# Kernel optimization log

Measured on AMD Instinct MI355X. Metric: run time of the kernel, lower is better.

## Reference

```python
import jax, jax.numpy as jnp
import numpy as np

B, S, T, D, H, HD = 1, 2048, 256, 3072, 24, 128
FF = 4 * D
EPS_LN = 1e-6
EPS_RMS = 1e-6


def _layernorm(x):
    m = jnp.mean(x, axis=-1, keepdims=True)
    v = jnp.mean(jnp.square(x - m), axis=-1, keepdims=True)
    return (x - m) * jax.lax.rsqrt(v + EPS_LN)


def _rmsnorm(x, w):
    return x * jax.lax.rsqrt(jnp.mean(jnp.square(x), axis=-1, keepdims=True) + EPS_RMS) * w


def _rope_interleaved(x, cos, sin):
    # x: [B,S,H,HD], cos/sin: [S,HD//2]; non-neox (interleaved) style
    x1 = x[..., 0::2]
    x2 = x[..., 1::2]
    c = cos[None, :, None, :]
    s = sin[None, :, None, :]
    o1 = x1 * c - x2 * s
    o2 = x2 * c + x1 * s
    return jnp.stack([o1, o2], axis=-1).reshape(x.shape)


def setup_inputs() -> dict:
    key = jax.random.key(0)
    ks = jax.random.split(key, 12)

    def n(k, shape, scale):
        return jax.random.normal(k, shape, dtype=jnp.float32) * scale

    # real RoPE tables
    pos = np.arange(S, dtype=np.float64)
    inv_freq = 1.0 / (10000.0 ** (np.arange(0, HD, 2, dtype=np.float64) / HD))
    ang = np.outer(pos, inv_freq)  # [S, HD//2]

    return {
        "img": n(ks[0], (B, S, D), 1.0),
        "vec": n(ks[1], (B, D), 1.0),
        "cos": jnp.asarray(np.cos(ang), jnp.float32),
        "sin": jnp.asarray(np.sin(ang), jnp.float32),
        "k_txt": n(ks[2], (B, T, H, HD), 1.0),
        "v_txt": n(ks[3], (B, T, H, HD), 1.0),
        "mod_w": n(ks[4], (D, 6 * D), 0.02),
        "mod_b": jnp.zeros((6 * D,), jnp.float32),
        "qkv_w": n(ks[5], (D, 3 * D), 0.02),
        "qkv_b": jnp.zeros((3 * D,), jnp.float32),
        "qn_w": jnp.ones((HD,), jnp.float32),
        "kn_w": jnp.ones((HD,), jnp.float32),
        "proj_w": n(ks[6], (D, D), 0.02),
        "proj_b": jnp.zeros((D,), jnp.float32),
        "mlp_w1": n(ks[7], (D, FF), 0.02),
        "mlp_b1": jnp.zeros((FF,), jnp.float32),
        "mlp_w2": n(ks[8], (FF, D), 0.02),
        "mlp_b2": jnp.zeros((D,), jnp.float32),
    }


def reference(img, vec, cos, sin, k_txt, v_txt, mod_w, mod_b, qkv_w, qkv_b,
              qn_w, kn_w, proj_w, proj_b, mlp_w1, mlp_b1, mlp_w2, mlp_b2):
    # modulation: silu(vec) -> linear -> 6 chunks, each [B,1,D]
    mod = jax.nn.silu(vec) @ mod_w + mod_b
    (a_shift, a_scale, a_gate, m_shift, m_scale, m_gate) = [
        m[:, None, :] for m in jnp.split(mod, 6, axis=-1)
    ]

    # LayerNorm (no affine) + scale/shift modulate
    x = _layernorm(img) * (1.0 + a_scale) + a_shift

    qkv = (x @ qkv_w + qkv_b).reshape(B, S, 3, H, HD)
    q, k, v = qkv[:, :, 0], qkv[:, :, 1], qkv[:, :, 2]
    q = _rmsnorm(q, qn_w)
    k = _rmsnorm(k, kn_w)
    q = _rope_interleaved(q, cos, sin)
    k = _rope_interleaved(k, cos, sin)

    # concat text KV cache (no RoPE on text tokens)
    k_all = jnp.concatenate([k, k_txt], axis=1)  # [B,S+T,H,HD]
    v_all = jnp.concatenate([v, v_txt], axis=1)

    scale = 1.0 / jnp.sqrt(jnp.asarray(HD, jnp.float32))
    scores = jnp.einsum('bqhd,bkhd->bhqk', q, k_all) * scale
    probs = jax.nn.softmax(scores, axis=-1)
    attn = jnp.einsum('bhqk,bkhd->bqhd', probs, v_all).reshape(B, S, D)

    attn_out = attn @ proj_w + proj_b

    # ScaleResidualLayerNormScaleShift
    residual = img + a_gate * attn_out
    mlp_in = _layernorm(residual) * (1.0 + m_scale) + m_shift

    mlp_out = jax.nn.gelu(mlp_in @ mlp_w1 + mlp_b1, approximate=True) @ mlp_w2 + mlp_b2
    return residual + m_gate * mlp_out
```

## Files before the change

kernel.cpp:

```cpp
#include <hip/hip_runtime.h>

typedef short short8 __attribute__((ext_vector_type(8)));
typedef float f32x4 __attribute__((ext_vector_type(4)));

#define DEV static __device__ __forceinline__

DEV unsigned short f2bf(float f) {
  union { float f; unsigned u; } v; v.f = f;
  unsigned u = v.u;
  unsigned r = u + 0x7fffu + ((u >> 16) & 1u);
  return (unsigned short)(r >> 16);
}
DEV float bf2f(unsigned short b) {
  union { unsigned u; float f; } v; v.u = ((unsigned)b) << 16;
  return v.f;
}
DEV void load_lds16(const void* g, void* l) {
  __builtin_amdgcn_global_load_lds(
      (const __attribute__((address_space(1))) unsigned int*)g,
      (__attribute__((address_space(3))) unsigned int*)l, 16, 0, 0);
}
DEV int swz(int L) { return L ^ ((L >> 3) & 0x30); }

__global__ __launch_bounds__(256) void zero_mod(const float* __restrict__ b, float* __restrict__ out) {
  int j = blockIdx.x * 256 + threadIdx.x;
  out[j] = b[j];
}

__global__ __launch_bounds__(256) void mod_gemv(const float* __restrict__ vec,
                                                const float* __restrict__ W,
                                                float* __restrict__ out) {
  __shared__ float sv[192];
  int tid = threadIdx.x;
  int kb = blockIdx.y * 192;
  if (tid < 192) {
    float x = vec[kb + tid];
    sv[tid] = x / (1.f + __expf(-x));
  }
  __syncthreads();
  int j = blockIdx.x * 256 + tid;
  float a0 = 0, a1 = 0, a2 = 0, a3 = 0;
  for (int i = 0; i < 192; i += 4) {
    a0 += sv[i + 0] * W[(size_t)(kb + i + 0) * 18432 + j];
    a1 += sv[i + 1] * W[(size_t)(kb + i + 1) * 18432 + j];
    a2 += sv[i + 2] * W[(size_t)(kb + i + 2) * 18432 + j];
    a3 += sv[i + 3] * W[(size_t)(kb + i + 3) * 18432 + j];
  }
  atomicAdd(&out[j], a0 + a1 + a2 + a3);
}

__global__ __launch_bounds__(256) void ln_kernel(const float* __restrict__ in,
                                                 const float* __restrict__ mod,
                                                 int shift_off, int scale_off,
                                                 unsigned short* __restrict__ out) {
  int rowb = blockIdx.x;
  const float* x = in + (size_t)rowb * 3072;
  int tid = threadIdx.x;
  float s = 0.f, ss = 0.f;
  float4 v[3];
#pragma unroll
  for (int r = 0; r < 3; r++) {
    v[r] = *(const float4*)&x[r * 1024 + tid * 4];
    s += v[r].x + v[r].y + v[r].z + v[r].w;
    ss += v[r].x * v[r].x + v[r].y * v[r].y + v[r].z * v[r].z + v[r].w * v[r].w;
  }
#pragma unroll
  for (int m = 32; m; m >>= 1) { s += __shfl_xor(s, m); ss += __shfl_xor(ss, m); }
  __shared__ float red[8];
  int w = tid >> 6, lane = tid & 63;
  if (lane == 0) { red[w] = s; red[4 + w] = ss; }
  __syncthreads();
  s = red[0] + red[1] + red[2] + red[3];
  ss = red[4] + red[5] + red[6] + red[7];
  float mean = s * (1.f / 3072.f);
  float var = ss * (1.f / 3072.f) - mean * mean;
  float rstd = rsqrtf(var + 1e-6f);
#pragma unroll
  for (int r = 0; r < 3; r++) {
    int c = r * 1024 + tid * 4;
    float xv[4] = {v[r].x, v[r].y, v[r].z, v[r].w};
#pragma unroll
    for (int i = 0; i < 4; i++) {
      float o = (xv[i] - mean) * rstd * (1.f + mod[scale_off + c + i]) + mod[shift_off + c + i];
      out[(size_t)rowb * 3072 + c + i] = f2bf(o);
    }
  }
}

__global__ __launch_bounds__(256) void transpose_k(const float* __restrict__ src,
                                                   unsigned short* __restrict__ dst,
                                                   int K, int N) {
  __shared__ float t[64][65];
  int n0 = blockIdx.x * 64, k0 = blockIdx.y * 64;
  int tid = threadIdx.x;
#pragma unroll
  for (int i = 0; i < 16; i++) {
    int lin = i * 256 + tid;
    int r = lin >> 6, c = lin & 63;
    t[r][c] = src[(size_t)(k0 + r) * N + n0 + c];
  }
  __syncthreads();
#pragma unroll
  for (int i = 0; i < 16; i++) {
    int lin = i * 256 + tid;
    int rn = lin >> 6, cn = lin & 63;
    dst[(size_t)(n0 + rn) * K + k0 + cn] = f2bf(t[cn][rn]);
  }
}

__global__ __launch_bounds__(256) void vt_k(const unsigned short* __restrict__ qkvb,
                                            const float* __restrict__ v_txt,
                                            unsigned short* __restrict__ vt) {
  int h = blockIdx.y;
  int c8 = blockIdx.x * 2 + (threadIdx.x >> 7);
  int d = threadIdx.x & 127;
  int kvb = c8 * 8;
  short8 o;
  if (kvb < 2048) {
#pragma unroll
    for (int j = 0; j < 8; j++)
      o[j] = (short)qkvb[(size_t)(kvb + j) * 9216 + 6144 + h * 128 + d];
  } else {
#pragma unroll
    for (int j = 0; j < 8; j++)
      o[j] = (short)f2bf(v_txt[((size_t)(kvb + j - 2048) * 24 + h) * 128 + d]);
  }
  *(short8*)&vt[((size_t)h * 128 + d) * 2304 + kvb] = o;
}

template <int EPI>
__global__ __launch_bounds__(512, 2) void gemm8(const unsigned short* __restrict__ A,
                                                const unsigned short* __restrict__ Bt,
                                                const float* __restrict__ bias,
                                                unsigned short* __restrict__ outb,
                                                int N, int ldk, int klen) {
  __shared__ unsigned short As[4][8192];
  __shared__ unsigned short Bs[4][8192];
  const int tid = threadIdx.x, lane = tid & 63, w = tid >> 6;
  const int wr = w >> 2, wc = w & 3;
  const int lr = lane & 15, lk = lane >> 4;

  const int bm = blockIdx.y * 256, bn = blockIdx.x * 256;
  const int kbase = blockIdx.z * klen;
  const int NT = klen >> 5;

  const int D0 = tid * 16;
  const int D1 = 8192 + tid * 16;
  const int L0 = swz(D0), L1 = swz(D1);
  const unsigned short* sA0 = A + (size_t)(bm + (L0 >> 6)) * ldk + kbase + ((L0 & 63) >> 1);
  const unsigned short* sA1 = A + (size_t)(bm + (L1 >> 6)) * ldk + kbase + ((L1 & 63) >> 1);
  const unsigned short* sB0 = Bt + (size_t)(bn + (L0 >> 6)) * ldk + kbase + ((L0 & 63) >> 1);
  const unsigned short* sB1 = Bt + (size_t)(bn + (L1 >> 6)) * ldk + kbase + ((L1 & 63) >> 1);

  int aoff[8], boff[4];
#pragma unroll
  for (int mi = 0; mi < 8; mi++)
    aoff[mi] = swz(((wr * 128 + mi * 16 + lr) << 6) | (lk << 4));
#pragma unroll
  for (int ni = 0; ni < 4; ni++)
    boff[ni] = swz(((wc * 64 + ni * 16 + lr) << 6) | (lk << 4));

  f32x4 acc[8][4];
#pragma unroll
  for (int i = 0; i < 8; i++)
#pragma unroll
    for (int j = 0; j < 4; j++) acc[i][j] = (f32x4){0.f, 0.f, 0.f, 0.f};

#pragma unroll
  for (int j = 0; j < 3; j++) {
    load_lds16(sA0 + j * 32, (char*)As + j * 16384 + D0);
    load_lds16(sA1 + j * 32, (char*)As + j * 16384 + D1);
    load_lds16(sB0 + j * 32, (char*)Bs + j * 16384 + D0);
    load_lds16(sB1 + j * 32, (char*)Bs + j * 16384 + D1);
  }
  asm volatile("s_waitcnt vmcnt(8)" ::: "memory");
  __builtin_amdgcn_sched_barrier(0);
  __builtin_amdgcn_s_barrier();

  for (int t = 0; t < NT; ++t) {
    const int rt = t & 3;
    char* Ab = (char*)As + rt * 16384;
    char* Bb = (char*)Bs + rt * 16384;
    const int ss = (t + 3) & 3;
    const int sk = (t + 3) * 32;
    const bool stg = (t + 3) < NT;

    short8 af[8], bf[4];
#pragma unroll
    for (int mi = 0; mi < 8; mi++) af[mi] = *(const short8*)(Ab + aoff[mi]);
#pragma unroll
    for (int ni = 0; ni < 4; ni++) bf[ni] = *(const short8*)(Bb + boff[ni]);
    if (stg) {
      load_lds16(sA0 + sk, (char*)As + ss * 16384 + D0);
      load_lds16(sA1 + sk, (char*)As + ss * 16384 + D1);
      load_lds16(sB0 + sk, (char*)Bs + ss * 16384 + D0);
      load_lds16(sB1 + sk, (char*)Bs + ss * 16384 + D1);
    }
    __builtin_amdgcn_s_setprio(1);
#pragma unroll
    for (int mi = 0; mi < 8; mi++)
#pragma unroll
      for (int ni = 0; ni < 4; ni++)
        acc[mi][ni] = __builtin_amdgcn_mfma_f32_16x16x32_bf16(af[mi], bf[ni], acc[mi][ni], 0, 0, 0);
    __builtin_amdgcn_s_setprio(0);
    if (t < NT - 3) {
      asm volatile("s_waitcnt vmcnt(8)" ::: "memory");
    } else if (t == NT - 3) {
      asm volatile("s_waitcnt vmcnt(4)" ::: "memory");
    } else if (t == NT - 2) {
      asm volatile("s_waitcnt vmcnt(0)" ::: "memory");
    }
    __builtin_amdgcn_sched_barrier(0);
    __builtin_amdgcn_s_barrier();
  }

  const size_t zoff = (size_t)blockIdx.z * ((size_t)2048 * N);
#pragma unroll
  for (int mi = 0; mi < 8; mi++) {
#pragma unroll
    for (int ni = 0; ni < 4; ni++) {
      int row0 = bm + wr * 128 + mi * 16 + lk * 4;
      int col = bn + wc * 64 + ni * 16 + lr;
#pragma unroll
      for (int r = 0; r < 4; r++) {
        float vv = acc[mi][ni][r];
        if (EPI == 0) {
          outb[(size_t)(row0 + r) * N + col] = f2bf(vv + bias[col]);
        } else if (EPI == 2) {
          float x = vv + bias[col];
          float y = 0.7978845608028654f * (x + 0.044715f * x * x * x);
          float th = 1.f - 2.f / (__expf(2.f * y) + 1.f);
          outb[(size_t)(row0 + r) * N + col] = f2bf(0.5f * x * (1.f + th));
        } else {
          outb[zoff + (size_t)(row0 + r) * N + col] = f2bf(vv);
        }
      }
    }
  }
}

__global__ __launch_bounds__(256) void sk_epi(const unsigned short* __restrict__ pb,
                                              const float* __restrict__ bias,
                                              const float* __restrict__ addsrc,
                                              const float* __restrict__ gate,
                                              float* __restrict__ out) {
  const int N = 3072;
  const size_t MN = (size_t)2048 * 3072;
  int row = blockIdx.y;
  int col = blockIdx.x * 1024 + threadIdx.x * 4;
  size_t idx = (size_t)row * N + col;
  const unsigned short* p0 = pb + idx;
  const unsigned short* p1 = pb + MN + idx;
  float4 a = *(const float4*)(addsrc + idx);
  float4 b = *(const float4*)(bias + col);
  float4 g = *(const float4*)(gate + col);
  float4 o;
  o.x = a.x + g.x * (bf2f(p0[0]) + bf2f(p1[0]) + b.x);
  o.y = a.y + g.y * (bf2f(p0[1]) + bf2f(p1[1]) + b.y);
  o.z = a.z + g.z * (bf2f(p0[2]) + bf2f(p1[2]) + b.z);
  o.w = a.w + g.w * (bf2f(p0[3]) + bf2f(p1[3]) + b.w);
  *(float4*)(out + idx) = o;
}

__global__ __launch_bounds__(64) void qkv_post(const unsigned short* __restrict__ qkv,
                                               const float* __restrict__ k_txt,
                                               const float* __restrict__ cosb,
                                               const float* __restrict__ sinb,
                                               const float* __restrict__ qn,
                                               const float* __restrict__ kn,
                                               unsigned short* __restrict__ qb,
                                               unsigned short* __restrict__ kb) {
  int s = blockIdx.x, h = blockIdx.y;
  int lane = threadIdx.x;
  int d0 = lane * 2;
  if (s < 2048) {
    const unsigned short* rowp = qkv + (size_t)s * 9216;
    float c = cosb[s * 64 + lane], sn = sinb[s * 64 + lane];
    const float ascale = 0.08838834764831845f;
    {
      float a = bf2f(rowp[h * 128 + d0]), b = bf2f(rowp[h * 128 + d0 + 1]);
      float sq = a * a + b * b;
#pragma unroll
      for (int m = 32; m; m >>= 1) sq += __shfl_xor(sq, m);
      float rr = rsqrtf(sq * (1.f / 128.f) + 1e-6f);
      float x1 = a * rr * qn[d0], x2 = b * rr * qn[d0 + 1];
      float o1 = (x1 * c - x2 * sn) * ascale;
      float o2 = (x2 * c + x1 * sn) * ascale;
      size_t off = ((size_t)h * 2048 + s) * 128 + d0;
      qb[off] = f2bf(o1); qb[off + 1] = f2bf(o2);
    }
    {
      float a = bf2f(rowp[3072 + h * 128 + d0]), b = bf2f(rowp[3072 + h * 128 + d0 + 1]);
      float sq = a * a + b * b;
#pragma unroll
      for (int m = 32; m; m >>= 1) sq += __shfl_xor(sq, m);
      float rr = rsqrtf(sq * (1.f / 128.f) + 1e-6f);
      float x1 = a * rr * kn[d0], x2 = b * rr * kn[d0 + 1];
      float o1 = x1 * c - x2 * sn;
      float o2 = x2 * c + x1 * sn;
      size_t off = ((size_t)h * 2304 + s) * 128 + d0;
      kb[off] = f2bf(o1); kb[off + 1] = f2bf(o2);
    }
  } else {
    int t = s - 2048;
    size_t src = ((size_t)t * 24 + h) * 128 + d0;
    size_t off = ((size_t)h * 2304 + s) * 128 + d0;
    kb[off] = f2bf(k_txt[src]); kb[off + 1] = f2bf(k_txt[src + 1]);
  }
}

__global__ __launch_bounds__(512) void attn_k(const unsigned short* __restrict__ qb,
                                              const unsigned short* __restrict__ kb,
                                              const unsigned short* __restrict__ vt,
                                              unsigned short* __restrict__ out) {
  __shared__ unsigned short Ks[2][8192];
  __shared__ unsigned short Vs[2][8192];
  __shared__ unsigned short Ps[8][32 * 72];
  int h = blockIdx.y, q0 = blockIdx.x * 256;
  int tid = threadIdx.x, lane = tid & 63, w = tid >> 6;
  int lr = lane & 15, lk = lane >> 4;

  const unsigned short* kh = kb + (size_t)h * 2304 * 128;
  const unsigned short* vth = vt + (size_t)h * 128 * 2304;

  short8 qf[2][4];
#pragma unroll
  for (int mi = 0; mi < 2; mi++)
#pragma unroll
    for (int kf = 0; kf < 4; kf++)
      qf[mi][kf] = *(const short8*)&qb[((size_t)h * 2048 + q0 + w * 32 + mi * 16 + lr) * 128 + kf * 32 + lk * 8];

  const int kR0 = (tid * 16) >> 8, kR1 = (tid * 16 + 8192) >> 8;
  const int kCc = ((tid * 16) >> 4) & 15;
  const int kOf0 = kR0 * 128 + ((kCc ^ (kR0 & 15)) * 8);
  const int kOf1 = kR1 * 128 + ((kCc ^ (kR1 & 15)) * 8);
  const int vR0 = (tid * 16) >> 7, vR1 = (tid * 16 + 8192) >> 7;
  const int vCc = ((tid * 16) >> 4) & 7;
  const int vOf0 = vR0 * 2304 + ((vCc ^ (vR0 & 7)) * 8);
  const int vOf1 = vR1 * 2304 + ((vCc ^ (vR1 & 7)) * 8);

  float mrow[2][4], lsum[2][4];
#pragma unroll
  for (int mi = 0; mi < 2; mi++)
#pragma unroll
    for (int r = 0; r < 4; r++) { mrow[mi][r] = -1e30f; lsum[mi][r] = 0.f; }
  f32x4 oacc[2][8];
#pragma unroll
  for (int mi = 0; mi < 2; mi++)
#pragma unroll
    for (int i = 0; i < 8; i++) oacc[mi][i] = (f32x4){0.f, 0.f, 0.f, 0.f};

  load_lds16(kh + kOf0, (char*)Ks[0] + tid * 16);
  load_lds16(kh + kOf1, (char*)Ks[0] + tid * 16 + 8192);
  load_lds16(vth + vOf0, (char*)Vs[0] + tid * 16);
  load_lds16(vth + vOf1, (char*)Vs[0] + tid * 16 + 8192);
  asm volatile("s_waitcnt vmcnt(0)" ::: "memory");
  __builtin_amdgcn_sched_barrier(0);
  __builtin_amdgcn_s_barrier();

  for (int kt = 0; kt < 36; kt++) {
    const int cur = kt & 1, nxt = cur ^ 1;
    if (kt + 1 < 36) {
      int kv1 = (kt + 1) * 64;
      load_lds16(kh + (size_t)kv1 * 128 + kOf0, (char*)Ks[nxt] + tid * 16);
      load_lds16(kh + (size_t)kv1 * 128 + kOf1, (char*)Ks[nxt] + tid * 16 + 8192);
      load_lds16(vth + kv1 + vOf0, (char*)Vs[nxt] + tid * 16);
      load_lds16(vth + kv1 + vOf1, (char*)Vs[nxt] + tid * 16 + 8192);
    }

    f32x4 sa[2][4];
#pragma unroll
    for (int mi = 0; mi < 2; mi++)
#pragma unroll
      for (int ni = 0; ni < 4; ni++) sa[mi][ni] = (f32x4){0.f, 0.f, 0.f, 0.f};
    __builtin_amdgcn_s_setprio(1);
#pragma unroll
    for (int kf = 0; kf < 4; kf++) {
#pragma unroll
      for (int ni = 0; ni < 4; ni++) {
        int n = ni * 16 + lr;
        short8 bfr = *(const short8*)&Ks[cur][n * 128 + (((kf * 4 + lk) ^ lr) & 15) * 8];
        sa[0][ni] = __builtin_amdgcn_mfma_f32_16x16x32_bf16(qf[0][kf], bfr, sa[0][ni], 0, 0, 0);
        sa[1][ni] = __builtin_amdgcn_mfma_f32_16x16x32_bf16(qf[1][kf], bfr, sa[1][ni], 0, 0, 0);
      }
    }
    __builtin_amdgcn_s_setprio(0);

#pragma unroll
    for (int mi = 0; mi < 2; mi++) {
#pragma unroll
      for (int r = 0; r < 4; r++) {
        float mx = fmaxf(fmaxf(sa[mi][0][r], sa[mi][1][r]), fmaxf(sa[mi][2][r], sa[mi][3][r]));
#pragma unroll
        for (int m = 8; m; m >>= 1) mx = fmaxf(mx, __shfl_xor(mx, m));
        float mnew = fmaxf(mrow[mi][r], mx);
        float p0 = __expf(sa[mi][0][r] - mnew);
        float p1 = __expf(sa[mi][1][r] - mnew);
        float p2 = __expf(sa[mi][2][r] - mnew);
        float p3 = __expf(sa[mi][3][r] - mnew);
        float su = p0 + p1 + p2 + p3;
#pragma unroll
        for (int m = 8; m; m >>= 1) su += __shfl_xor(su, m);
        float alpha = __expf(mrow[mi][r] - mnew);
        lsum[mi][r] = lsum[mi][r] * alpha + su;
        mrow[mi][r] = mnew;
#pragma unroll
        for (int df = 0; df < 8; df++) oacc[mi][df][r] *= alpha;
        int prow = (mi * 16 + lk * 4 + r) * 72;
        Ps[w][prow + 0 * 16 + lr] = f2bf(p0);
        Ps[w][prow + 1 * 16 + lr] = f2bf(p1);
        Ps[w][prow + 2 * 16 + lr] = f2bf(p2);
        Ps[w][prow + 3 * 16 + lr] = f2bf(p3);
      }
    }

    __builtin_amdgcn_s_setprio(1);
#pragma unroll
    for (int kf2 = 0; kf2 < 2; kf2++) {
      short8 pa0 = *(const short8*)&Ps[w][(0 * 16 + lr) * 72 + kf2 * 32 + lk * 8];
      short8 pa1 = *(const short8*)&Ps[w][(1 * 16 + lr) * 72 + kf2 * 32 + lk * 8];
#pragma unroll
      for (int df = 0; df < 8; df++) {
        int d = df * 16 + lr;
        short8 bv = *(const short8*)&Vs[cur][d * 64 + (((kf2 * 4 + lk) ^ (lr & 7)) & 7) * 8];
        oacc[0][df] = __builtin_amdgcn_mfma_f32_16x16x32_bf16(pa0, bv, oacc[0][df], 0, 0, 0);
        oacc[1][df] = __builtin_amdgcn_mfma_f32_16x16x32_bf16(pa1, bv, oacc[1][df], 0, 0, 0);
      }
    }
    __builtin_amdgcn_s_setprio(0);

    asm volatile("s_waitcnt vmcnt(0)" ::: "memory");
    __builtin_amdgcn_sched_barrier(0);
    __builtin_amdgcn_s_barrier();
  }

#pragma unroll
  for (int mi = 0; mi < 2; mi++) {
#pragma unroll
    for (int r = 0; r < 4; r++) {
      float inv = 1.f / lsum[mi][r];
      int row = q0 + w * 32 + mi * 16 + lk * 4 + r;
#pragma unroll
      for (int df = 0; df < 8; df++)
        out[(size_t)row * 3072 + h * 128 + df * 16 + lr] = f2bf(oacc[mi][df][r] * inv);
    }
  }
}

extern "C" void kernel_launch(void* const* d_in, const int* in_sizes, int n_in,
                              void* d_out, int out_size, void* d_ws, size_t ws_size,
                              hipStream_t stream) {
  const float* img = (const float*)d_in[0];
  const float* vec = (const float*)d_in[1];
  const float* cosb = (const float*)d_in[2];
  const float* sinb = (const float*)d_in[3];
  const float* k_txt = (const float*)d_in[4];
  const float* v_txt = (const float*)d_in[5];
  const float* mod_w = (const float*)d_in[6];
  const float* mod_b = (const float*)d_in[7];
  const float* qkv_w = (const float*)d_in[8];
  const float* qkv_b = (const float*)d_in[9];
  const float* qn_w = (const float*)d_in[10];
  const float* kn_w = (const float*)d_in[11];
  const float* proj_w = (const float*)d_in[12];
  const float* proj_b = (const float*)d_in[13];
  const float* mlp_w1 = (const float*)d_in[14];
  const float* mlp_b1 = (const float*)d_in[15];
  const float* mlp_w2 = (const float*)d_in[16];
  const float* mlp_b2 = (const float*)d_in[17];
  float* outp = (float*)d_out;

  char* ws = (char*)d_ws;
  unsigned short* qkvb = (unsigned short*)(ws + 0);
  unsigned short* qbuf = (unsigned short*)(ws + 37748736);
  unsigned short* kbuf = (unsigned short*)(ws + 50331648);
  unsigned short* vtbuf = (unsigned short*)(ws + 64487424);
  unsigned short* attnb = (unsigned short*)(ws + 78643200);
  float* resid = (float*)(ws + 91226112);
  unsigned short* xln = (unsigned short*)(ws + 116391936);
  float* modv = (float*)(ws + 128974848);
  unsigned short* wt = (unsigned short*)(ws + 129048576);
  unsigned short* hbuf = (unsigned short*)(ws + 0);
  unsigned short* pbuf = (unsigned short*)(ws + 50331648);

  zero_mod<<<72, 256, 0, stream>>>(mod_b, modv);
  mod_gemv<<<dim3(72, 16), 256, 0, stream>>>(vec, mod_w, modv);

  ln_kernel<<<2048, 256, 0, stream>>>(img, modv, 0, 3072, xln);

  transpose_k<<<dim3(144, 48), 256, 0, stream>>>(qkv_w, wt, 3072, 9216);
  gemm8<0><<<dim3(36, 8, 1), 512, 0, stream>>>(xln, wt, qkv_b, qkvb, 9216, 3072, 3072);

  qkv_post<<<dim3(2304, 24), 64, 0, stream>>>(qkvb, k_txt, cosb, sinb, qn_w, kn_w, qbuf, kbuf);
  vt_k<<<dim3(144, 24), 256, 0, stream>>>(qkvb, v_txt, vtbuf);

  attn_k<<<dim3(8, 24), 512, 0, stream>>>(qbuf, kbuf, vtbuf, attnb);

  transpose_k<<<dim3(48, 48), 256, 0, stream>>>(proj_w, wt, 3072, 3072);
  gemm8<3><<<dim3(12, 8, 2), 512, 0, stream>>>(attnb, wt, nullptr, pbuf, 3072, 3072, 1536);
  sk_epi<<<dim3(3, 2048), 256, 0, stream>>>(pbuf, proj_b, img, modv + 2 * 3072, resid);

  ln_kernel<<<2048, 256, 0, stream>>>(resid, modv, 3 * 3072, 4 * 3072, xln);

  transpose_k<<<dim3(192, 48), 256, 0, stream>>>(mlp_w1, wt, 3072, 12288);
  gemm8<2><<<dim3(48, 8, 1), 512, 0, stream>>>(xln, wt, mlp_b1, hbuf, 12288, 3072, 3072);

  transpose_k<<<dim3(48, 192), 256, 0, stream>>>(mlp_w2, wt, 12288, 3072);
  gemm8<3><<<dim3(12, 8, 2), 512, 0, stream>>>(hbuf, wt, nullptr, pbuf, 3072, 12288, 6144);
  sk_epi<<<dim3(3, 2048), 256, 0, stream>>>(pbuf, mlp_b2, resid, modv + 5 * 3072, outp);
}
```

Measured before the change: 958.2 us.

## Double-buffer GEMM fragments in registers to overlap LDS reads with MFMA

Restructures the gemm8 main loop into a two-step unrolled pipeline. It keeps two sets of A/B fragment registers and reads the next tile's fragments from LDS while the MFMAs for the current tile run. Prefetch issue and vmcnt waits are reorganised so each tile only waits on the tile it needs next. The aim is to hide LDS read latency behind matrix-core work. The cost is extra fragment VGPRs, which could cause spills or lower occupancy under the 512x2 launch bounds. The loop also assumes an even tile count.

```diff
diff --git a/kernel.cpp b/kernel.cpp
--- a/kernel.cpp
+++ b/kernel.cpp
@@ -127,6 +127,48 @@
   }
   *(short8*)&vt[((size_t)h * 128 + d) * 2304 + kvb] = o;
 }
+
+#define RD_FRAGS(AF, BF, Ab, Bb)                                   \
+  do {                                                             \
+    _Pragma("unroll")                                              \
+    for (int mi = 0; mi < 8; mi++) AF[mi] = *(const short8*)((Ab) + aoff[mi]); \
+    _Pragma("unroll")                                              \
+    for (int ni = 0; ni < 4; ni++) BF[ni] = *(const short8*)((Bb) + boff[ni]); \
+  } while (0)
+
+#define DO_MFMA(AF, BF)                                            \
+  do {                                                             \
+    __builtin_amdgcn_s_setprio(1);                                 \
+    _Pragma("unroll")                                              \
+    for (int mi = 0; mi < 8; mi++)                                 \
+      _Pragma("unroll")                                            \
+      for (int ni = 0; ni < 4; ni++)                               \
+        acc[mi][ni] = __builtin_amdgcn_mfma_f32_16x16x32_bf16(AF[mi], BF[ni], acc[mi][ni], 0, 0, 0); \
+    __builtin_amdgcn_s_setprio(0);                                 \
+  } while (0)
+
+#define STAGE4(TT)                                                 \
+  do {                                                             \
+    if ((TT) < NT) {                                               \
+      const int ss_ = (TT) & 3;                                    \
+      const int sk_ = (TT) * 32;                                   \
+      load_lds16(sA0 + sk_, (char*)As + ss_ * 16384 + D0);         \
+      load_lds16(sA1 + sk_, (char*)As + ss_ * 16384 + D1);         \
+      load_lds16(sB0 + sk_, (char*)Bs + ss_ * 16384 + D0);         \
+      load_lds16(sB1 + sk_, (char*)Bs + ss_ * 16384 + D1);         \
+    }                                                              \
+  } while (0)
+
+#define TILE_WAIT(U)                                               \
+  do {                                                             \
+    if ((U) <= NT - 4) {                                           \
+      asm volatile("s_waitcnt vmcnt(4)" ::: "memory");             \
+    } else {                                                       \
+      asm volatile("s_waitcnt vmcnt(0)" ::: "memory");             \
+    }                                                              \
+    __builtin_amdgcn_sched_barrier(0);                             \
+    __builtin_amdgcn_s_barrier();                                  \
+  } while (0)
 
 template <int EPI>
 __global__ __launch_bounds__(512, 2) void gemm8(const unsigned short* __restrict__ A,
@@ -166,52 +208,35 @@
 #pragma unroll
     for (int j = 0; j < 4; j++) acc[i][j] = (f32x4){0.f, 0.f, 0.f, 0.f};
 
-#pragma unroll
-  for (int j = 0; j < 3; j++) {
-    load_lds16(sA0 + j * 32, (char*)As + j * 16384 + D0);
-    load_lds16(sA1 + j * 32, (char*)As + j * 16384 + D1);
-    load_lds16(sB0 + j * 32, (char*)Bs + j * 16384 + D0);
-    load_lds16(sB1 + j * 32, (char*)Bs + j * 16384 + D1);
-  }
-  asm volatile("s_waitcnt vmcnt(8)" ::: "memory");
+  STAGE4(0);
+  STAGE4(1);
+  STAGE4(2);
+  asm volatile("s_waitcnt vmcnt(4)" ::: "memory");
   __builtin_amdgcn_sched_barrier(0);
   __builtin_amdgcn_s_barrier();
 
-  for (int t = 0; t < NT; ++t) {
-    const int rt = t & 3;
-    char* Ab = (char*)As + rt * 16384;
-    char* Bb = (char*)Bs + rt * 16384;
-    const int ss = (t + 3) & 3;
-    const int sk = (t + 3) * 32;
-    const bool stg = (t + 3) < NT;
-
-    short8 af[8], bf[4];
-#pragma unroll
-    for (int mi = 0; mi < 8; mi++) af[mi] = *(const short8*)(Ab + aoff[mi]);
-#pragma unroll
-    for (int ni = 0; ni < 4; ni++) bf[ni] = *(const short8*)(Bb + boff[ni]);
-    if (stg) {
-      load_lds16(sA0 + sk, (char*)As + ss * 16384 + D0);
-      load_lds16(sA1 + sk, (char*)As + ss * 16384 + D1);
-      load_lds16(sB0 + sk, (char*)Bs + ss * 16384 + D0);
-      load_lds16(sB1 + sk, (char*)Bs + ss * 16384 + D1);
-    }
-    __builtin_amdgcn_s_setprio(1);
-#pragma unroll
-    for (int mi = 0; mi < 8; mi++)
-#pragma unroll
-      for (int ni = 0; ni < 4; ni++)
-        acc[mi][ni] = __builtin_amdgcn_mfma_f32_16x16x32_bf16(af[mi], bf[ni], acc[mi][ni], 0, 0, 0);
-    __builtin_amdgcn_s_setprio(0);
-    if (t < NT - 3) {
-      asm volatile("s_waitcnt vmcnt(8)" ::: "memory");
-    } else if (t == NT - 3) {
-      asm volatile("s_waitcnt vmcnt(4)" ::: "memory");
-    } else if (t == NT - 2) {
-      asm volatile("s_waitcnt vmcnt(0)" ::: "memory");
-    }
-    __builtin_amdgcn_sched_barrier(0);
-    __builtin_amdgcn_s_barrier();
+  short8 afA[8], bfA[4], afB[8], bfB[4];
+  RD_FRAGS(afA, bfA, (char*)As, (char*)Bs);
+
+  for (int t = 0; t < NT; t += 2) {
+    {
+      STAGE4(t + 3);
+      char* Ab = (char*)As + ((t + 1) & 3) * 16384;
+      char* Bb = (char*)Bs + ((t + 1) & 3) * 16384;
+      RD_FRAGS(afB, bfB, Ab, Bb);
+      DO_MFMA(afA, bfA);
+      TILE_WAIT(t);
+    }
+    {
+      STAGE4(t + 4);
+      if (t + 2 < NT) {
+        char* Ab = (char*)As + ((t + 2) & 3) * 16384;
+        char* Bb = (char*)Bs + ((t + 2) & 3) * 16384;
+        RD_FRAGS(afA, bfA, Ab, Bb);
+      }
+      DO_MFMA(afB, bfB);
+      TILE_WAIT(t + 1);
+    }
   }
 
   const size_t zoff = (size_t)blockIdx.z * ((size_t)2048 * N);
```

New measurement: 1.170 ms. 1.22x slower.

## Rework GEMM to double-buffered K64 tiles and add split-K for QKV and MLP2

Applied to the files above, without the earlier changes.

The GEMM main loop moves from a 4-stage ring of 32-wide K tiles to a 2-stage double buffer of 64-wide K tiles, with a new XOR swizzle on 128-byte rows. The goal is fewer barriers and waits per unit of MFMA work, but only one tile is now prefetched ahead, which hides less memory latency. The QKV projection becomes a 2-way split-K GEMM followed by a new bf16 reduction kernel that adds the bias. The MLP down projection goes from a 2-way to a 3-way split-K, and the epilogue is templated on the number of splits. Both split-K changes raise the block count for better CU fill, at the cost of extra partial-sum traffic and an added kernel launch.

```diff
diff --git a/kernel.cpp b/kernel.cpp
--- a/kernel.cpp
+++ b/kernel.cpp
@@ -20,7 +20,6 @@
       (const __attribute__((address_space(1))) unsigned int*)g,
       (__attribute__((address_space(3))) unsigned int*)l, 16, 0, 0);
 }
-DEV int swz(int L) { return L ^ ((L >> 3) & 0x30); }
 
 __global__ __launch_bounds__(256) void zero_mod(const float* __restrict__ b, float* __restrict__ out) {
   int j = blockIdx.x * 256 + threadIdx.x;
@@ -133,32 +132,41 @@
                                                 const unsigned short* __restrict__ Bt,
                                                 const float* __restrict__ bias,
                                                 unsigned short* __restrict__ outb,
-                                                int N, int ldk, int klen) {
-  __shared__ unsigned short As[4][8192];
-  __shared__ unsigned short Bs[4][8192];
+                                                int N, int ldk, int klen, size_t zstride) {
+  __shared__ unsigned short As[2][16384];
+  __shared__ unsigned short Bs[2][16384];
   const int tid = threadIdx.x, lane = tid & 63, w = tid >> 6;
   const int wr = w >> 2, wc = w & 3;
   const int lr = lane & 15, lk = lane >> 4;
 
   const int bm = blockIdx.y * 256, bn = blockIdx.x * 256;
   const int kbase = blockIdx.z * klen;
-  const int NT = klen >> 5;
-
-  const int D0 = tid * 16;
-  const int D1 = 8192 + tid * 16;
-  const int L0 = swz(D0), L1 = swz(D1);
-  const unsigned short* sA0 = A + (size_t)(bm + (L0 >> 6)) * ldk + kbase + ((L0 & 63) >> 1);
-  const unsigned short* sA1 = A + (size_t)(bm + (L1 >> 6)) * ldk + kbase + ((L1 & 63) >> 1);
-  const unsigned short* sB0 = Bt + (size_t)(bn + (L0 >> 6)) * ldk + kbase + ((L0 & 63) >> 1);
-  const unsigned short* sB1 = Bt + (size_t)(bn + (L1 >> 6)) * ldk + kbase + ((L1 & 63) >> 1);
+  const int NT = klen >> 6;
+
+  const unsigned short* sA[4];
+  const unsigned short* sB[4];
+  int Dd[4];
+#pragma unroll
+  for (int j = 0; j < 4; j++) {
+    int D = j * 8192 + tid * 16;
+    int row = D >> 7;
+    int sw = ((D >> 4) & 7) ^ (row & 7);
+    Dd[j] = D;
+    sA[j] = A + (size_t)(bm + row) * ldk + kbase + sw * 8;
+    sB[j] = Bt + (size_t)(bn + row) * ldk + kbase + sw * 8;
+  }
 
   int aoff[8], boff[4];
 #pragma unroll
-  for (int mi = 0; mi < 8; mi++)
-    aoff[mi] = swz(((wr * 128 + mi * 16 + lr) << 6) | (lk << 4));
-#pragma unroll
-  for (int ni = 0; ni < 4; ni++)
-    boff[ni] = swz(((wc * 64 + ni * 16 + lr) << 6) | (lk << 4));
+  for (int mi = 0; mi < 8; mi++) {
+    int r = wr * 128 + mi * 16 + lr;
+    aoff[mi] = r * 128 + ((lk ^ (r & 7)) << 4);
+  }
+#pragma unroll
+  for (int ni = 0; ni < 4; ni++) {
+    int r = wc * 64 + ni * 16 + lr;
+    boff[ni] = r * 128 + ((lk ^ (r & 7)) << 4);
+  }
 
   f32x4 acc[8][4];
 #pragma unroll
@@ -167,54 +175,49 @@
     for (int j = 0; j < 4; j++) acc[i][j] = (f32x4){0.f, 0.f, 0.f, 0.f};
 
 #pragma unroll
-  for (int j = 0; j < 3; j++) {
-    load_lds16(sA0 + j * 32, (char*)As + j * 16384 + D0);
-    load_lds16(sA1 + j * 32, (char*)As + j * 16384 + D1);
-    load_lds16(sB0 + j * 32, (char*)Bs + j * 16384 + D0);
-    load_lds16(sB1 + j * 32, (char*)Bs + j * 16384 + D1);
-  }
-  asm volatile("s_waitcnt vmcnt(8)" ::: "memory");
+  for (int j = 0; j < 4; j++) {
+    load_lds16(sA[j], (char*)As + Dd[j]);
+    load_lds16(sB[j], (char*)Bs + Dd[j]);
+  }
+  asm volatile("s_waitcnt vmcnt(0)" ::: "memory");
   __builtin_amdgcn_sched_barrier(0);
   __builtin_amdgcn_s_barrier();
 
   for (int t = 0; t < NT; ++t) {
-    const int rt = t & 3;
-    char* Ab = (char*)As + rt * 16384;
-    char* Bb = (char*)Bs + rt * 16384;
-    const int ss = (t + 3) & 3;
-    const int sk = (t + 3) * 32;
-    const bool stg = (t + 3) < NT;
-
-    short8 af[8], bf[4];
-#pragma unroll
-    for (int mi = 0; mi < 8; mi++) af[mi] = *(const short8*)(Ab + aoff[mi]);
-#pragma unroll
-    for (int ni = 0; ni < 4; ni++) bf[ni] = *(const short8*)(Bb + boff[ni]);
-    if (stg) {
-      load_lds16(sA0 + sk, (char*)As + ss * 16384 + D0);
-      load_lds16(sA1 + sk, (char*)As + ss * 16384 + D1);
-      load_lds16(sB0 + sk, (char*)Bs + ss * 16384 + D0);
-      load_lds16(sB1 + sk, (char*)Bs + ss * 16384 + D1);
-    }
-    __builtin_amdgcn_s_setprio(1);
-#pragma unroll
-    for (int mi = 0; mi < 8; mi++)
-#pragma unroll
-      for (int ni = 0; ni < 4; ni++)
-        acc[mi][ni] = __builtin_amdgcn_mfma_f32_16x16x32_bf16(af[mi], bf[ni], acc[mi][ni], 0, 0, 0);
-    __builtin_amdgcn_s_setprio(0);
-    if (t < NT - 3) {
-      asm volatile("s_waitcnt vmcnt(8)" ::: "memory");
-    } else if (t == NT - 3) {
-      asm volatile("s_waitcnt vmcnt(4)" ::: "memory");
-    } else if (t == NT - 2) {
-      asm volatile("s_waitcnt vmcnt(0)" ::: "memory");
-    }
+    const int ct = t & 1;
+    char* Ab = (char*)As + ct * 32768;
+    char* Bb = (char*)Bs + ct * 32768;
+    if (t + 1 < NT) {
+      char* Ad = (char*)As + (ct ^ 1) * 32768;
+      char* Bd = (char*)Bs + (ct ^ 1) * 32768;
+      int ko = (t + 1) * 64;
+#pragma unroll
+      for (int j = 0; j < 4; j++) {
+        load_lds16(sA[j] + ko, Ad + Dd[j]);
+        load_lds16(sB[j] + ko, Bd + Dd[j]);
+      }
+    }
+#pragma unroll
+    for (int kk = 0; kk < 2; kk++) {
+      short8 af[8], bf[4];
+#pragma unroll
+      for (int mi = 0; mi < 8; mi++) af[mi] = *(const short8*)(Ab + (aoff[mi] ^ (kk << 6)));
+#pragma unroll
+      for (int ni = 0; ni < 4; ni++) bf[ni] = *(const short8*)(Bb + (boff[ni] ^ (kk << 6)));
+      __builtin_amdgcn_s_setprio(1);
+#pragma unroll
+      for (int mi = 0; mi < 8; mi++)
+#pragma unroll
+        for (int ni = 0; ni < 4; ni++)
+          acc[mi][ni] = __builtin_amdgcn_mfma_f32_16x16x32_bf16(af[mi], bf[ni], acc[mi][ni], 0, 0, 0);
+      __builtin_amdgcn_s_setprio(0);
+    }
+    asm volatile("s_waitcnt vmcnt(0)" ::: "memory");
     __builtin_amdgcn_sched_barrier(0);
     __builtin_amdgcn_s_barrier();
   }
 
-  const size_t zoff = (size_t)blockIdx.z * ((size_t)2048 * N);
+  const size_t zoff = (size_t)blockIdx.z * zstride;
 #pragma unroll
   for (int mi = 0; mi < 8; mi++) {
 #pragma unroll
@@ -239,6 +242,7 @@
   }
 }
 
+template <int NS>
 __global__ __launch_bounds__(256) void sk_epi(const unsigned short* __restrict__ pb,
                                               const float* __restrict__ bias,
                                               const float* __restrict__ addsrc,
@@ -249,17 +253,35 @@
   int row = blockIdx.y;
   int col = blockIdx.x * 1024 + threadIdx.x * 4;
   size_t idx = (size_t)row * N + col;
-  const unsigned short* p0 = pb + idx;
-  const unsigned short* p1 = pb + MN + idx;
   float4 a = *(const float4*)(addsrc + idx);
   float4 b = *(const float4*)(bias + col);
   float4 g = *(const float4*)(gate + col);
+  float sum[4] = {b.x, b.y, b.z, b.w};
+#pragma unroll
+  for (int s = 0; s < NS; s++) {
+    const unsigned short* p = pb + s * MN + idx;
+#pragma unroll
+    for (int i = 0; i < 4; i++) sum[i] += bf2f(p[i]);
+  }
   float4 o;
-  o.x = a.x + g.x * (bf2f(p0[0]) + bf2f(p1[0]) + b.x);
-  o.y = a.y + g.y * (bf2f(p0[1]) + bf2f(p1[1]) + b.y);
-  o.z = a.z + g.z * (bf2f(p0[2]) + bf2f(p1[2]) + b.z);
-  o.w = a.w + g.w * (bf2f(p0[3]) + bf2f(p1[3]) + b.w);
+  o.x = a.x + g.x * sum[0];
+  o.y = a.y + g.y * sum[1];
+  o.z = a.z + g.z * sum[2];
+  o.w = a.w + g.w * sum[3];
   *(float4*)(out + idx) = o;
+}
+
+__global__ __launch_bounds__(256) void sk_epiq(const unsigned short* __restrict__ p0,
+                                               const unsigned short* __restrict__ p1,
+                                               const float* __restrict__ bias,
+                                               unsigned short* __restrict__ out) {
+  const int N = 9216;
+  int row = blockIdx.y;
+  int col = blockIdx.x * 1024 + threadIdx.x * 4;
+  size_t idx = (size_t)row * N + col;
+#pragma unroll
+  for (int i = 0; i < 4; i++)
+    out[idx + i] = f2bf(bf2f(p0[idx + i]) + bf2f(p1[idx + i]) + bias[col + i]);
 }
 
 __global__ __launch_bounds__(64) void qkv_post(const unsigned short* __restrict__ qkv,
@@ -470,6 +492,7 @@
   const float* mlp_b2 = (const float*)d_in[17];
   float* outp = (float*)d_out;
 
+  const size_t MN = (size_t)2048 * 3072;
   char* ws = (char*)d_ws;
   unsigned short* qkvb = (unsigned short*)(ws + 0);
   unsigned short* qbuf = (unsigned short*)(ws + 37748736);
@@ -481,6 +504,9 @@
   float* modv = (float*)(ws + 128974848);
   unsigned short* wt = (unsigned short*)(ws + 129048576);
   unsigned short* hbuf = (unsigned short*)(ws + 0);
+  unsigned short* qp0 = (unsigned short*)(ws + 37748736);
+  const size_t qzstride = (78643200 - 37748736) / 2;
+  unsigned short* qp1 = (unsigned short*)(ws + 78643200);
   unsigned short* pbuf = (unsigned short*)(ws + 50331648);
 
   zero_mod<<<72, 256, 0, stream>>>(mod_b, modv);
@@ -489,7 +515,8 @@
   ln_kernel<<<2048, 256, 0, stream>>>(img, modv, 0, 3072, xln);
 
   transpose_k<<<dim3(144, 48), 256, 0, stream>>>(qkv_w, wt, 3072, 9216);
-  gemm8<0><<<dim3(36, 8, 1), 512, 0, stream>>>(xln, wt, qkv_b, qkvb, 9216, 3072, 3072);
+  gemm8<3><<<dim3(36, 8, 2), 512, 0, stream>>>(xln, wt, nullptr, qp0, 9216, 3072, 1536, qzstride);
+  sk_epiq<<<dim3(9, 2048), 256, 0, stream>>>(qp0, qp1, qkv_b, qkvb);
 
   qkv_post<<<dim3(2304, 24), 64, 0, stream>>>(qkvb, k_txt, cosb, sinb, qn_w, kn_w, qbuf, kbuf);
   vt_k<<<dim3(144, 24), 256, 0, stream>>>(qkvb, v_txt, vtbuf);
@@ -497,15 +524,15 @@
   attn_k<<<dim3(8, 24), 512, 0, stream>>>(qbuf, kbuf, vtbuf, attnb);
 
   transpose_k<<<dim3(48, 48), 256, 0, stream>>>(proj_w, wt, 3072, 3072);
-  gemm8<3><<<dim3(12, 8, 2), 512, 0, stream>>>(attnb, wt, nullptr, pbuf, 3072, 3072, 1536);
-  sk_epi<<<dim3(3, 2048), 256, 0, stream>>>(pbuf, proj_b, img, modv + 2 * 3072, resid);
+  gemm8<3><<<dim3(12, 8, 2), 512, 0, stream>>>(attnb, wt, nullptr, pbuf, 3072, 3072, 1536, MN);
+  sk_epi<2><<<dim3(3, 2048), 256, 0, stream>>>(pbuf, proj_b, img, modv + 2 * 3072, resid);
 
   ln_kernel<<<2048, 256, 0, stream>>>(resid, modv, 3 * 3072, 4 * 3072, xln);
 
   transpose_k<<<dim3(192, 48), 256, 0, stream>>>(mlp_w1, wt, 3072, 12288);
-  gemm8<2><<<dim3(48, 8, 1), 512, 0, stream>>>(xln, wt, mlp_b1, hbuf, 12288, 3072, 3072);
+  gemm8<2><<<dim3(48, 8, 1), 512, 0, stream>>>(xln, wt, mlp_b1, hbuf, 12288, 3072, 3072, 0);
 
   transpose_k<<<dim3(48, 192), 256, 0, stream>>>(mlp_w2, wt, 12288, 3072);
-  gemm8<3><<<dim3(12, 8, 2), 512, 0, stream>>>(hbuf, wt, nullptr, pbuf, 3072, 12288, 6144);
-  sk_epi<<<dim3(3, 2048), 256, 0, stream>>>(pbuf, mlp_b2, resid, modv + 5 * 3072, outp);
-}
+  gemm8<3><<<dim3(12, 8, 3), 512, 0, stream>>>(hbuf, wt, nullptr, pbuf, 3072, 12288, 4096, MN);
+  sk_epi<3><<<dim3(3, 2048), 256, 0, stream>>>(pbuf, mlp_b2, resid, modv + 5 * 3072, outp);
+}
```

New measurement: 1.134 ms. 1.18x slower.
